# Kernel tuning notes

Measured on AMD Instinct MI355X. Metric: run time of the kernel, lower is better.

The kernel has to match this reference:

```python
import jax, jax.numpy as jnp
import numpy as np

Z = 20000      # batch (e.g., graph nodes)
U = 128        # segment multiplicity ('u' mode)
S = 8          # segments per operand (same for all 4 operands here)
P = 64         # number of paths


def setup_inputs() -> dict:
    key = jax.random.key(0)
    k0, k1, k2, kc, ki = jax.random.split(key, 5)
    x0 = jax.random.normal(k0, (Z, S * U), dtype=jnp.float32)
    x1 = jax.random.normal(k1, (Z, S * U), dtype=jnp.float32)
    x2 = jax.random.normal(k2, (Z, S * U), dtype=jnp.float32)
    path_coefficients = jax.random.normal(kc, (P,), dtype=jnp.float32)
    # each path picks one segment index per operand (op0, op1, op2, output)
    path_indices = jax.random.randint(ki, (P, 4), 0, S, dtype=jnp.int32)
    return {"x0": x0, "x1": x1, "x2": x2,
            "path_coefficients": path_coefficients,
            "path_indices": path_indices}


def reference(x0, x1, x2, path_coefficients, path_indices):
    # Segmented tensor product, channelwise mode 'u,u,u->u':
    # out[z, i3, u] += sum_p c[p] * x0[z, i0[p], u] * x1[z, i1[p], u] * x2[z, i2[p], u]
    x0s = x0.reshape(Z, S, U)
    x1s = x1.reshape(Z, S, U)
    x2s = x2.reshape(Z, S, U)
    i0, i1, i2, i3 = (path_indices[:, 0], path_indices[:, 1],
                      path_indices[:, 2], path_indices[:, 3])
    # gather segments per path: [Z, P, U]
    prod = (x0s[:, i0, :] * x1s[:, i1, :] * x2s[:, i2, :]
            * path_coefficients[None, :, None])
    # scatter-add paths into output segments: [S, Z, U]
    out = jax.ops.segment_sum(jnp.swapaxes(prod, 0, 1), i3, num_segments=S)
    return jnp.swapaxes(out, 0, 1).reshape(Z, S * U)
```

## Files before the change

### kernel.cpp

```cpp
#include <hip/hip_runtime.h>

constexpr int Zn = 20000;
constexpr int Un = 128;
constexpr int Sn = 8;
constexpr int Pn = 64;
constexpr int ROW = Sn * Un;
constexpr int ZPB = 2;
constexpr int THREADS = 256;

__global__ __launch_bounds__(64) void prep_kernel(const int* __restrict__ pi,
                                                  const float* __restrict__ pc,
                                                  int4* __restrict__ table,
                                                  int* __restrict__ segstart) {
    const int p = threadIdx.x & 63;
    const int i0 = pi[4 * p + 0];
    const int i1 = pi[4 * p + 1];
    const int i2 = pi[4 * p + 2];
    const int i3 = pi[4 * p + 3];
    const float w = pc[p];
    const unsigned long long below = (1ull << p) - 1ull;

    int base = 0, slot = 0;
#pragma unroll
    for (int s = 0; s < Sn; ++s) {
        unsigned long long m = __ballot(i3 == s);
        if (i3 == s) slot = base + __popcll(m & below);
        if (p == 0) segstart[s] = base;
        base += __popcll(m);
    }
    if (p == 0) segstart[Sn] = base;

    table[slot] = make_int4(i0 * Un,
                            ZPB * ROW + i1 * Un,
                            2 * ZPB * ROW + i2 * Un,
                            __float_as_int(w));
}

__global__ __launch_bounds__(THREADS, 6) void tp_kernel(
        const float* __restrict__ x0,
        const float* __restrict__ x1,
        const float* __restrict__ x2,
        const int4* __restrict__ table,
        const int* __restrict__ segstart,
        float* __restrict__ out) {
    __shared__ __align__(16) float lds[3 * ZPB * ROW];
    const int tid = threadIdx.x;
    const int zblk = blockIdx.x * ZPB;

#pragma unroll
    for (int t = 0; t < 3; ++t) {
        const float4* src = (const float4*)(t == 0 ? x0 : (t == 1 ? x1 : x2));
        float4* dst = (float4*)lds + t * (ZPB * ROW / 4);
#pragma unroll
        for (int i = 0; i < (ZPB * ROW / 4) / THREADS; ++i) {
            int local = i * THREADS + tid;
            int z = local >> 8;
            int r = local & 255;
            dst[local] = src[(size_t)(zblk + z) * (ROW / 4) + r];
        }
    }

    const int lane = tid & 63;
    const int wave = tid >> 6;
    const int zloc = lane >> 5;
    const int u4   = lane & 31;
    const int s0   = wave * 2;

    const int kbeg = segstart[s0];
    const int kmid = segstart[s0 + 1];
    const int kend = segstart[s0 + 2];

    __syncthreads();

    const float* zb = lds + zloc * ROW;
    float4 acc0 = make_float4(0.f, 0.f, 0.f, 0.f);
    float4 acc1 = make_float4(0.f, 0.f, 0.f, 0.f);

    int4 e = table[__builtin_amdgcn_readfirstlane(kbeg < kend ? kbeg : 0)];
    for (int k = kbeg; k < kend; ++k) {
        const int kn = (k + 1 < kend) ? k + 1 : k;
        const int4 en = table[__builtin_amdgcn_readfirstlane(kn)];

        const float4 a = *(const float4*)(zb + e.x + u4 * 4);
        const float4 b = *(const float4*)(zb + e.y + u4 * 4);
        const float4 c = *(const float4*)(zb + e.z + u4 * 4);
        const float w  = __int_as_float(e.w);
        const float w0 = (k < kmid) ? w : 0.f;
        const float w1 = (k < kmid) ? 0.f : w;

        float4 p;
        p.x = a.x * b.x * c.x;
        p.y = a.y * b.y * c.y;
        p.z = a.z * b.z * c.z;
        p.w = a.w * b.w * c.w;
        acc0.x = fmaf(p.x, w0, acc0.x);
        acc0.y = fmaf(p.y, w0, acc0.y);
        acc0.z = fmaf(p.z, w0, acc0.z);
        acc0.w = fmaf(p.w, w0, acc0.w);
        acc1.x = fmaf(p.x, w1, acc1.x);
        acc1.y = fmaf(p.y, w1, acc1.y);
        acc1.z = fmaf(p.z, w1, acc1.z);
        acc1.w = fmaf(p.w, w1, acc1.w);

        e = en;
    }

    float* orow = out + (size_t)(zblk + zloc) * ROW;
    *(float4*)(orow + s0 * Un + u4 * 4) = acc0;
    *(float4*)(orow + (s0 + 1) * Un + u4 * 4) = acc1;
}

extern "C" void kernel_launch(void* const* d_in, const int* in_sizes, int n_in,
                              void* d_out, int out_size, void* d_ws, size_t ws_size,
                              hipStream_t stream) {
    const float* x0 = (const float*)d_in[0];
    const float* x1 = (const float*)d_in[1];
    const float* x2 = (const float*)d_in[2];
    const float* pc = (const float*)d_in[3];
    const int*   pi = (const int*)d_in[4];
    float* out = (float*)d_out;

    int4* table    = (int4*)d_ws;
    int*  segstart = (int*)((char*)d_ws + Pn * sizeof(int4));

    prep_kernel<<<1, 64, 0, stream>>>(pi, pc, table, segstart);
    tp_kernel<<<Zn / ZPB, THREADS, 0, stream>>>(x0, x1, x2, table, segstart, out);
}
```

Measured before the change: 260.6 us.

## Use persistent blocks with register-staged prefetch of the next z-pair

The kernel becomes persistent with a fixed grid of 1536 blocks that loop over z-pairs. While computing on the current pair in LDS, each block loads the next pair's inputs from global into registers, then writes them to LDS after a barrier. The inner loop also software-pipelines its LDS reads by one path. The goal is to hide global load latency behind compute, at the cost of more registers and an extra barrier per iteration.

```diff
diff --git a/kernel.cpp b/kernel.cpp
--- a/kernel.cpp
+++ b/kernel.cpp
@@ -6,7 +6,9 @@
 constexpr int Pn = 64;
 constexpr int ROW = Sn * Un;
 constexpr int ZPB = 2;
+constexpr int NZP = Zn / ZPB;
 constexpr int THREADS = 256;
+constexpr int GRID = 1536;
 
 __global__ __launch_bounds__(64) void prep_kernel(const int* __restrict__ pi,
                                                   const float* __restrict__ pc,
@@ -44,22 +46,7 @@
         const int* __restrict__ segstart,
         float* __restrict__ out) {
     __shared__ __align__(16) float lds[3 * ZPB * ROW];
-    const int tid = threadIdx.x;
-    const int zblk = blockIdx.x * ZPB;
-
-#pragma unroll
-    for (int t = 0; t < 3; ++t) {
-        const float4* src = (const float4*)(t == 0 ? x0 : (t == 1 ? x1 : x2));
-        float4* dst = (float4*)lds + t * (ZPB * ROW / 4);
-#pragma unroll
-        for (int i = 0; i < (ZPB * ROW / 4) / THREADS; ++i) {
-            int local = i * THREADS + tid;
-            int z = local >> 8;
-            int r = local & 255;
-            dst[local] = src[(size_t)(zblk + z) * (ROW / 4) + r];
-        }
-    }
-
+    const int tid  = threadIdx.x;
     const int lane = tid & 63;
     const int wave = tid >> 6;
     const int zloc = lane >> 5;
@@ -70,44 +57,91 @@
     const int kmid = segstart[s0 + 1];
     const int kend = segstart[s0 + 2];
 
+    const float* zb = lds + zloc * ROW;
+
+    float4 st[6];
+
+    auto LOAD = [&](int zp) {
+#pragma unroll
+        for (int t = 0; t < 3; ++t) {
+            const float4* src = (const float4*)(t == 0 ? x0 : (t == 1 ? x1 : x2));
+#pragma unroll
+            for (int i = 0; i < 2; ++i) {
+                const int local = i * THREADS + tid;
+                const int z = local >> 8;
+                const int r = local & 255;
+                st[t * 2 + i] = src[(size_t)(zp * ZPB + z) * (ROW / 4) + r];
+            }
+        }
+    };
+    auto WRITE = [&]() {
+#pragma unroll
+        for (int t = 0; t < 3; ++t) {
+            float4* dst = (float4*)lds + t * (ZPB * ROW / 4);
+#pragma unroll
+            for (int i = 0; i < 2; ++i) {
+                const int local = i * THREADS + tid;
+                dst[local] = st[t * 2 + i];
+            }
+        }
+    };
+
+    int zp = blockIdx.x;
+    LOAD(zp);
+    WRITE();
     __syncthreads();
 
-    const float* zb = lds + zloc * ROW;
-    float4 acc0 = make_float4(0.f, 0.f, 0.f, 0.f);
-    float4 acc1 = make_float4(0.f, 0.f, 0.f, 0.f);
+    for (;;) {
+        const int zpn = zp + (int)gridDim.x;
+        const bool more = zpn < NZP;
+        if (more) LOAD(zpn);
 
-    int4 e = table[__builtin_amdgcn_readfirstlane(kbeg < kend ? kbeg : 0)];
-    for (int k = kbeg; k < kend; ++k) {
-        const int kn = (k + 1 < kend) ? k + 1 : k;
-        const int4 en = table[__builtin_amdgcn_readfirstlane(kn)];
+        float4 acc0 = make_float4(0.f, 0.f, 0.f, 0.f);
+        float4 acc1 = make_float4(0.f, 0.f, 0.f, 0.f);
 
-        const float4 a = *(const float4*)(zb + e.x + u4 * 4);
-        const float4 b = *(const float4*)(zb + e.y + u4 * 4);
-        const float4 c = *(const float4*)(zb + e.z + u4 * 4);
-        const float w  = __int_as_float(e.w);
-        const float w0 = (k < kmid) ? w : 0.f;
-        const float w1 = (k < kmid) ? 0.f : w;
+        int4 e0 = table[__builtin_amdgcn_readfirstlane(kbeg < kend ? kbeg : 0)];
+        float4 a0 = *(const float4*)(zb + e0.x + u4 * 4);
+        float4 b0 = *(const float4*)(zb + e0.y + u4 * 4);
+        float4 c0 = *(const float4*)(zb + e0.z + u4 * 4);
 
-        float4 p;
-        p.x = a.x * b.x * c.x;
-        p.y = a.y * b.y * c.y;
-        p.z = a.z * b.z * c.z;
-        p.w = a.w * b.w * c.w;
-        acc0.x = fmaf(p.x, w0, acc0.x);
-        acc0.y = fmaf(p.y, w0, acc0.y);
-        acc0.z = fmaf(p.z, w0, acc0.z);
-        acc0.w = fmaf(p.w, w0, acc0.w);
-        acc1.x = fmaf(p.x, w1, acc1.x);
-        acc1.y = fmaf(p.y, w1, acc1.y);
-        acc1.z = fmaf(p.z, w1, acc1.z);
-        acc1.w = fmaf(p.w, w1, acc1.w);
+        for (int k = kbeg; k < kend; ++k) {
+            const int kn = (k + 1 < kend) ? k + 1 : k;
+            const int4 e1 = table[__builtin_amdgcn_readfirstlane(kn)];
+            const float4 a1 = *(const float4*)(zb + e1.x + u4 * 4);
+            const float4 b1 = *(const float4*)(zb + e1.y + u4 * 4);
+            const float4 c1 = *(const float4*)(zb + e1.z + u4 * 4);
 
-        e = en;
+            const float w  = __int_as_float(e0.w);
+            const float w0 = (k < kmid) ? w : 0.f;
+            const float w1 = w - w0;
+
+            float4 p;
+            p.x = a0.x * b0.x * c0.x;
+            p.y = a0.y * b0.y * c0.y;
+            p.z = a0.z * b0.z * c0.z;
+            p.w = a0.w * b0.w * c0.w;
+            acc0.x = fmaf(p.x, w0, acc0.x);
+            acc0.y = fmaf(p.y, w0, acc0.y);
+            acc0.z = fmaf(p.z, w0, acc0.z);
+            acc0.w = fmaf(p.w, w0, acc0.w);
+            acc1.x = fmaf(p.x, w1, acc1.x);
+            acc1.y = fmaf(p.y, w1, acc1.y);
+            acc1.z = fmaf(p.z, w1, acc1.z);
+            acc1.w = fmaf(p.w, w1, acc1.w);
+
+            e0 = e1; a0 = a1; b0 = b1; c0 = c1;
+        }
+
+        float* orow = out + (size_t)(zp * ZPB + zloc) * ROW;
+        *(float4*)(orow + s0 * Un + u4 * 4) = acc0;
+        *(float4*)(orow + (s0 + 1) * Un + u4 * 4) = acc1;
+
+        __syncthreads();
+        if (!more) break;
+        WRITE();
+        __syncthreads();
+        zp = zpn;
     }
-
-    float* orow = out + (size_t)(zblk + zloc) * ROW;
-    *(float4*)(orow + s0 * Un + u4 * 4) = acc0;
-    *(float4*)(orow + (s0 + 1) * Un + u4 * 4) = acc1;
 }
 
 extern "C" void kernel_launch(void* const* d_in, const int* in_sizes, int n_in,
@@ -124,5 +158,5 @@
     int*  segstart = (int*)((char*)d_ws + Pn * sizeof(int4));
 
     prep_kernel<<<1, 64, 0, stream>>>(pi, pc, table, segstart);
-    tp_kernel<<<Zn / ZPB, THREADS, 0, stream>>>(x0, x1, x2, table, segstart, out);
+    tp_kernel<<<GRID, THREADS, 0, stream>>>(x0, x1, x2, table, segstart, out);
 }
```

Measured after the change: 294.9 us. 13.2% more time.
